# Performance work log

Hardware: AMD Instinct MI355X
Metric: run time of the kernel (lower is better)

## Reference

```python
import jax, jax.numpy as jnp
import numpy as np

EMB = 1024
HEAD = 64

def setup_inputs() -> dict:
    key = jax.random.key(0)
    kx, kq, kk, kv = jax.random.split(key, 4)
    x = jax.random.normal(kx, (8, 2048, EMB), dtype=jnp.float32)
    # nn.Linear(emb, head, bias=False): y = x @ W.T, W: [head, emb]. Store as [emb, head].
    s = 1.0 / np.sqrt(EMB)
    Wq = jax.random.uniform(kq, (EMB, HEAD), jnp.float32, -s, s)
    Wk = jax.random.uniform(kk, (EMB, HEAD), jnp.float32, -s, s)
    Wv = jax.random.uniform(kv, (EMB, HEAD), jnp.float32, -s, s)
    return {"x": x, "Wq": Wq, "Wk": Wk, "Wv": Wv}

def reference(x, Wq, Wk, Wv):
    B, T, C = x.shape
    q = x @ Wq  # [B,T,H]
    k = x @ Wk
    v = x @ Wv
    # NOTE: original scales by emb_size C, not head_size.
    wei = jnp.einsum('bth,bsh->bts', q, k) / jnp.sqrt(jnp.asarray(C, x.dtype))
    causal = jnp.tril(jnp.ones((T, T), dtype=bool))
    wei = jnp.where(causal, wei, -jnp.inf)
    wei = jax.nn.softmax(wei, axis=-1)
    return jnp.einsum('bts,bsh->bth', wei, v)
```

## Files before the change

### kernel.cpp

```cpp
#include <hip/hip_runtime.h>
#include <hip/hip_bf16.h>

typedef __bf16 bf16_t;
typedef __bf16 bf16x8 __attribute__((ext_vector_type(8)));
typedef __bf16 bf16x4 __attribute__((ext_vector_type(4)));
typedef float  f32x4  __attribute__((ext_vector_type(4)));

#define MFMA_BF16(A, B, C) __builtin_amdgcn_mfma_f32_16x16x32_bf16((A), (B), (C), 0, 0, 0)

#define BATCH 8
#define SEQ   2048
#define EMB   1024
#define HEAD  64

typedef __attribute__((address_space(3))) void as3_void;
typedef const __attribute__((address_space(1))) void as1_void;
#define GLOAD_LDS16(g, l) \
  __builtin_amdgcn_global_load_lds((as1_void*)(g), (as3_void*)(l), 16, 0, 0)

__global__ __launch_bounds__(256) void wtrans_kernel(
    const float* __restrict__ Wq, const float* __restrict__ Wk,
    const float* __restrict__ Wv, bf16_t* __restrict__ WT)
{
  __shared__ float tile[64][65];
  const int m  = blockIdx.x >> 4;
  const int kt = blockIdx.x & 15;
  const float* W = (m == 0) ? Wq : (m == 1) ? Wk : Wv;
  const float scale = (m == 0) ? 0.045084219f : 1.0f;
  const int k0 = kt * 64;

  #pragma unroll
  for (int i = 0; i < 16; ++i) {
    int idx = i * 256 + threadIdx.x;
    int kk = idx >> 6, n = idx & 63;
    tile[kk][n] = W[(size_t)(k0 + kk) * HEAD + n];
  }
  __syncthreads();
  #pragma unroll
  for (int i = 0; i < 16; ++i) {
    int idx = i * 256 + threadIdx.x;
    int n = idx >> 6, kk = idx & 63;
    WT[((size_t)m * HEAD + n) * EMB + k0 + kk] = (bf16_t)(tile[kk][n] * scale);
  }
}

#define A_BYTES 16384
#define B_BYTES 24576
#define BUF_BYTES 40960

__global__ __launch_bounds__(512, 1) void qkv_kernel(
    const float* __restrict__ x, const bf16_t* __restrict__ WT,
    bf16_t* __restrict__ qo, bf16_t* __restrict__ ko, bf16_t* __restrict__ vT)
{
  __shared__ char lds[4 * BUF_BYTES];

  const int tid  = threadIdx.x;
  const int lane = tid & 63;
  const int wave = tid >> 6;
  const int l15 = lane & 15, l4 = lane >> 4;
  const int wm = wave >> 2, wn = wave & 3;
  const int rowbase = blockIdx.x * 64;
  const int phase = (blockIdx.x >> 3) & 15;

  const int a_rsub = lane >> 4;
  const int b_rsub = lane >> 3;
  const int b_koff = ((lane & 7) * 16) ^ (b_rsub << 4);

  const int aswz = (l15 & 7) << 5;
  const int bswz = (l15 & 7) << 4;

  f32x4 acc[2][3];
  #pragma unroll
  for (int m = 0; m < 2; ++m)
    #pragma unroll
    for (int n = 0; n < 3; ++n) acc[m][n] = (f32x4){0.f, 0.f, 0.f, 0.f};

#define STAGE(t)                                                               \
  {                                                                            \
    char* buf = lds + ((t) & 3) * BUF_BYTES;                                   \
    const int tp = ((t) + phase) & 15;                                         \
    _Pragma("unroll")                                                          \
    for (int j = 0; j < 2; ++j) {                                              \
      const int g = 2 * wave + j;                                              \
      const int koff = (l15 * 16) ^ ((((j) << 2) | a_rsub) << 5);              \
      const char* src = (const char*)x + (size_t)(rowbase + 4 * g + a_rsub)    \
                        * 4096 + (size_t)tp * 256 + koff;                      \
      GLOAD_LDS16(src, buf + g * 1024);                                        \
    }                                                                          \
    _Pragma("unroll")                                                          \
    for (int j = 0; j < 3; ++j) {                                              \
      const int g = 3 * wave + j;                                              \
      const char* src = (const char*)WT + (size_t)(8 * g + b_rsub) * 2048      \
                        + (size_t)tp * 128 + b_koff;                           \
      GLOAD_LDS16(src, buf + A_BYTES + g * 1024);                              \
    }                                                                          \
  }

#define COMPUTE(t)                                                             \
  {                                                                            \
    const char* Ab = lds + ((t) & 3) * BUF_BYTES;                              \
    const char* Bb = Ab + A_BYTES;                                             \
    _Pragma("unroll")                                                          \
    for (int ks = 0; ks < 2; ++ks) {                                           \
      bf16x8 afr[2];                                                           \
      _Pragma("unroll")                                                        \
      for (int m = 0; m < 2; ++m) {                                            \
        const int R = wm * 32 + m * 16 + l15;                                  \
        const char* rp = Ab + R * 256 + ((ks * 128 + l4 * 32) ^ aswz);         \
        f32x4 p0 = *(const f32x4*)(rp);                                        \
        f32x4 p1 = *(const f32x4*)(rp + 16);                                   \
        bf16x8 a;                                                              \
        a[0] = (bf16_t)p0.x; a[1] = (bf16_t)p0.y;                              \
        a[2] = (bf16_t)p0.z; a[3] = (bf16_t)p0.w;                              \
        a[4] = (bf16_t)p1.x; a[5] = (bf16_t)p1.y;                              \
        a[6] = (bf16_t)p1.z; a[7] = (bf16_t)p1.w;                              \
        afr[m] = a;                                                            \
      }                                                                        \
      _Pragma("unroll")                                                        \
      for (int n = 0; n < 3; ++n) {                                            \
        const int Rb = wn * 48 + n * 16 + l15;                                 \
        bf16x8 b = *(const bf16x8*)(Bb + Rb * 128 + ((ks * 64 + l4 * 16) ^ bswz)); \
        acc[0][n] = MFMA_BF16(afr[0], b, acc[0][n]);                           \
        acc[1][n] = MFMA_BF16(afr[1], b, acc[1][n]);                           \
      }                                                                        \
    }                                                                          \
  }

  STAGE(0); STAGE(1); STAGE(2);
  asm volatile("s_waitcnt vmcnt(10)" ::: "memory");
  __builtin_amdgcn_s_barrier();

  for (int t = 0; t < 13; ++t) {
    COMPUTE(t);
    STAGE(t + 3);
    asm volatile("s_waitcnt vmcnt(10)" ::: "memory");
    __builtin_amdgcn_s_barrier();
  }
  COMPUTE(13);
  asm volatile("s_waitcnt vmcnt(5)" ::: "memory");
  __builtin_amdgcn_s_barrier();
  COMPUTE(14);
  asm volatile("s_waitcnt vmcnt(0)" ::: "memory");
  __builtin_amdgcn_s_barrier();
  COMPUTE(15);
#undef STAGE
#undef COMPUTE

  #pragma unroll
  for (int n = 0; n < 3; ++n) {
    const int col = wn * 48 + n * 16;
    #pragma unroll
    for (int m = 0; m < 2; ++m) {
      const int r0 = rowbase + wm * 32 + m * 16 + l4 * 4;
      if (col < 64) {
        #pragma unroll
        for (int i = 0; i < 4; ++i)
          qo[(size_t)(r0 + i) * HEAD + col + l15] = (bf16_t)acc[m][n][i];
      } else if (col < 128) {
        #pragma unroll
        for (int i = 0; i < 4; ++i)
          ko[(size_t)(r0 + i) * HEAD + col - 64 + l15] = (bf16_t)acc[m][n][i];
      } else {
        const int h = col - 128 + l15;
        bf16x4 pk;
        #pragma unroll
        for (int i = 0; i < 4; ++i) pk[i] = (bf16_t)acc[m][n][i];
        *(bf16x4*)(vT + ((size_t)(r0 >> 11) * HEAD + h) * SEQ + (r0 & 2047)) = pk;
      }
    }
  }
}

__global__ __launch_bounds__(512, 1) void attn_kernel(
    const bf16_t* __restrict__ q, const bf16_t* __restrict__ k,
    const bf16_t* __restrict__ vT, float* __restrict__ out)
{
  __shared__ bf16_t P[8][16][72];
  __shared__ float olds[8][16][65];
  __shared__ float lsums[8][16];
  const int lane = threadIdx.x & 63;
  const int wave = threadIdx.x >> 6;
  const int l15 = lane & 15, l4 = lane >> 4;
  const int batch = blockIdx.x & 7;
  const int pair  = blockIdx.x >> 3;
  const int side  = wave >> 2;
  const int wsub  = wave & 3;
  const int strip = side ? (127 - pair) : pair;
  const int qrow  = strip * 16;
  const int ntiles = (qrow >> 6) + 1;

  const bf16_t* kb = k  + (size_t)batch * SEQ * HEAD;
  const bf16_t* vb = vT + (size_t)batch * HEAD * SEQ;
  const bf16_t* qb = q  + ((size_t)batch * SEQ + qrow) * HEAD;

  const bf16x8 aq0 = *(const bf16x8*)(qb + (size_t)l15 * HEAD + l4 * 8);
  const bf16x8 aq1 = *(const bf16x8*)(qb + (size_t)l15 * HEAD + 32 + l4 * 8);

  f32x4 o[4];
  #pragma unroll
  for (int i = 0; i < 4; ++i) o[i] = (f32x4){0.f, 0.f, 0.f, 0.f};
  float lsum[4] = {0.f, 0.f, 0.f, 0.f};

  for (int t = wsub; t < ntiles; t += 4) {
    const int kv0 = t * 64;

    f32x4 s[4];
    #pragma unroll
    for (int nf = 0; nf < 4; ++nf) s[nf] = (f32x4){0.f, 0.f, 0.f, 0.f};
    __builtin_amdgcn_s_setprio(1);
    #pragma unroll
    for (int nf = 0; nf < 4; ++nf) {
      const bf16_t* kp = kb + (size_t)(kv0 + nf * 16 + l15) * HEAD + l4 * 8;
      bf16x8 b0 = *(const bf16x8*)kp;
      bf16x8 b1 = *(const bf16x8*)(kp + 32);
      s[nf] = MFMA_BF16(aq0, b0, s[nf]);
      s[nf] = MFMA_BF16(aq1, b1, s[nf]);
    }
    __builtin_amdgcn_s_setprio(0);

    const bool diag = (t == ntiles - 1);
    #pragma unroll
    for (int nf = 0; nf < 4; ++nf) {
      #pragma unroll
      for (int i2 = 0; i2 < 4; ++i2) {
        float e = exp2f(s[nf][i2]);
        if (diag) {
          const int col = kv0 + nf * 16 + l15;
          const int row = qrow + l4 * 4 + i2;
          e = (col <= row) ? e : 0.f;
        }
        lsum[i2] += e;
        P[wave][l4 * 4 + i2][nf * 16 + l15] = (bf16_t)e;
      }
    }

    bf16x8 v0[4], v1[4];
    #pragma unroll
    for (int nf = 0; nf < 4; ++nf) {
      const bf16_t* vp = vb + (size_t)(nf * 16 + l15) * SEQ + kv0 + l4 * 8;
      v0[nf] = *(const bf16x8*)vp;
      v1[nf] = *(const bf16x8*)(vp + 32);
    }
    asm volatile("s_waitcnt lgkmcnt(0)" ::: "memory");

    bf16x8 ap0 = *(const bf16x8*)&P[wave][l15][l4 * 8];
    bf16x8 ap1 = *(const bf16x8*)&P[wave][l15][32 + l4 * 8];
    __builtin_amdgcn_s_setprio(1);
    #pragma unroll
    for (int nf = 0; nf < 4; ++nf) {
      o[nf] = MFMA_BF16(ap0, v0[nf], o[nf]);
      o[nf] = MFMA_BF16(ap1, v1[nf], o[nf]);
    }
    __builtin_amdgcn_s_setprio(0);
  }

  #pragma unroll
  for (int i = 0; i < 4; ++i) {
    float v = lsum[i];
    v += __shfl_xor(v, 1);
    v += __shfl_xor(v, 2);
    v += __shfl_xor(v, 4);
    v += __shfl_xor(v, 8);
    if (l15 == 0) lsums[wave][l4 * 4 + i] = v;
  }
  #pragma unroll
  for (int nf = 0; nf < 4; ++nf)
    #pragma unroll
    for (int i = 0; i < 4; ++i)
      olds[wave][l4 * 4 + i][nf * 16 + l15] = o[nf][i];
  __syncthreads();

  {
    const int g  = threadIdx.x >> 8;
    const int tt = threadIdx.x & 255;
    const int r = tt >> 4, c0 = tt & 15;
    const int sstrip = g ? (127 - pair) : pair;
    const int w0 = g * 4;
    const float s = lsums[w0][r] + lsums[w0+1][r] + lsums[w0+2][r] + lsums[w0+3][r];
    const float rinv = 1.0f / s;
    float* ob = out + ((size_t)batch * SEQ + sstrip * 16 + r) * HEAD;
    #pragma unroll
    for (int j = 0; j < 4; ++j) {
      const int c = c0 + 16 * j;
      float v = olds[w0][r][c] + olds[w0+1][r][c] + olds[w0+2][r][c] + olds[w0+3][r][c];
      ob[c] = v * rinv;
    }
  }
}

extern "C" void kernel_launch(void* const* d_in, const int* in_sizes, int n_in,
                              void* d_out, int out_size, void* d_ws, size_t ws_size,
                              hipStream_t stream)
{
  const float* x  = (const float*)d_in[0];
  const float* Wq = (const float*)d_in[1];
  const float* Wk = (const float*)d_in[2];
  const float* Wv = (const float*)d_in[3];
  float* out = (float*)d_out;

  const size_t SZ_QKV = (size_t)BATCH * SEQ * HEAD * sizeof(bf16_t);
  if (ws_size < 3 * SZ_QKV + (size_t)192 * EMB * sizeof(bf16_t)) return;
  char* ws = (char*)d_ws;
  bf16_t* qo = (bf16_t*)(ws);
  bf16_t* ko = (bf16_t*)(ws + SZ_QKV);
  bf16_t* vT = (bf16_t*)(ws + 2 * SZ_QKV);
  bf16_t* WT = (bf16_t*)(ws + 3 * SZ_QKV);

  wtrans_kernel<<<dim3(48),  dim3(256), 0, stream>>>(Wq, Wk, Wv, WT);
  qkv_kernel  <<<dim3(256), dim3(512), 0, stream>>>(x, WT, qo, ko, vT);
  attn_kernel <<<dim3(512), dim3(512), 0, stream>>>(qo, ko, vT, out);
}
```

Before: 56.57 us.

## Share K tiles across waves via triple-buffered LDS and drop split-KV reduction

The attention kernel now gives each block four consecutive query strips, one per wave, and each wave walks every KV tile itself. K tiles are staged into a swizzled, triple-buffered LDS ring with global_load_lds, so the four waves share one K load per tile. The old split-KV scheme with cross-wave LDS reduction and the front/back strip pairing is removed. Output is normalised and written straight from registers. This cuts redundant K global traffic and the reduction step, but each wave's KV loop becomes serial and longer. Without pairing, blocks become strongly imbalanced, and only 256 blocks of 4 waves are launched, which lowers occupancy.

```diff
diff --git a/kernel.cpp b/kernel.cpp
--- a/kernel.cpp
+++ b/kernel.cpp
@@ -171,23 +171,20 @@
   }
 }
 
-__global__ __launch_bounds__(512, 1) void attn_kernel(
+__global__ __launch_bounds__(256) void attn_kernel(
     const bf16_t* __restrict__ q, const bf16_t* __restrict__ k,
     const bf16_t* __restrict__ vT, float* __restrict__ out)
 {
-  __shared__ bf16_t P[8][16][72];
-  __shared__ float olds[8][16][65];
-  __shared__ float lsums[8][16];
+  __shared__ char kbuf[3][8192];
+  __shared__ bf16_t P[4][16][72];
   const int lane = threadIdx.x & 63;
   const int wave = threadIdx.x >> 6;
   const int l15 = lane & 15, l4 = lane >> 4;
   const int batch = blockIdx.x & 7;
-  const int pair  = blockIdx.x >> 3;
-  const int side  = wave >> 2;
-  const int wsub  = wave & 3;
-  const int strip = side ? (127 - pair) : pair;
+  const int u = (int)(blockIdx.x >> 3);
+  const int strip = 4 * u + wave;
   const int qrow  = strip * 16;
-  const int ntiles = (qrow >> 6) + 1;
+  const int ntiles = u + 1;
 
   const bf16_t* kb = k  + (size_t)batch * SEQ * HEAD;
   const bf16_t* vb = vT + (size_t)batch * HEAD * SEQ;
@@ -196,13 +193,34 @@
   const bf16x8 aq0 = *(const bf16x8*)(qb + (size_t)l15 * HEAD + l4 * 8);
   const bf16x8 aq1 = *(const bf16x8*)(qb + (size_t)l15 * HEAD + 32 + l4 * 8);
 
+  const int b_rsub = lane >> 3;
+  const int b_koff = ((lane & 7) * 16) ^ (b_rsub << 4);
+  const int kswz = (l15 & 7) << 4;
+
+#define KSTAGE(t)                                                              \
+  {                                                                            \
+    char* buf = kbuf[(t) % 3];                                                 \
+    _Pragma("unroll")                                                          \
+    for (int j = 0; j < 2; ++j) {                                              \
+      const int g = 2 * wave + j;                                              \
+      const char* src = (const char*)kb + (size_t)((t) * 64 + 8 * g + b_rsub)  \
+                        * 128 + b_koff;                                        \
+      GLOAD_LDS16(src, buf + g * 1024);                                        \
+    }                                                                          \
+  }
+
   f32x4 o[4];
   #pragma unroll
   for (int i = 0; i < 4; ++i) o[i] = (f32x4){0.f, 0.f, 0.f, 0.f};
   float lsum[4] = {0.f, 0.f, 0.f, 0.f};
 
-  for (int t = wsub; t < ntiles; t += 4) {
+  KSTAGE(0); KSTAGE(1);
+  asm volatile("s_waitcnt vmcnt(2)" ::: "memory");
+  __builtin_amdgcn_s_barrier();
+
+  for (int t = 0; t < ntiles; ++t) {
     const int kv0 = t * 64;
+    const char* Kb = kbuf[t % 3];
 
     f32x4 s[4];
     #pragma unroll
@@ -210,13 +228,23 @@
     __builtin_amdgcn_s_setprio(1);
     #pragma unroll
     for (int nf = 0; nf < 4; ++nf) {
-      const bf16_t* kp = kb + (size_t)(kv0 + nf * 16 + l15) * HEAD + l4 * 8;
-      bf16x8 b0 = *(const bf16x8*)kp;
-      bf16x8 b1 = *(const bf16x8*)(kp + 32);
+      const char* kr = (const char*)Kb + (nf * 16 + l15) * 128;
+      bf16x8 b0 = *(const bf16x8*)(kr + ((l4 * 16) ^ kswz));
+      bf16x8 b1 = *(const bf16x8*)(kr + ((64 + l4 * 16) ^ kswz));
       s[nf] = MFMA_BF16(aq0, b0, s[nf]);
       s[nf] = MFMA_BF16(aq1, b1, s[nf]);
     }
     __builtin_amdgcn_s_setprio(0);
+
+    bf16x8 v0[4], v1[4];
+    #pragma unroll
+    for (int nf = 0; nf < 4; ++nf) {
+      const bf16_t* vp = vb + (size_t)(nf * 16 + l15) * SEQ + kv0 + l4 * 8;
+      v0[nf] = *(const bf16x8*)vp;
+      v1[nf] = *(const bf16x8*)(vp + 32);
+    }
+
+    if (t + 2 < ntiles) KSTAGE(t + 2);
 
     const bool diag = (t == ntiles - 1);
     #pragma unroll
@@ -234,17 +262,11 @@
       }
     }
 
-    bf16x8 v0[4], v1[4];
-    #pragma unroll
-    for (int nf = 0; nf < 4; ++nf) {
-      const bf16_t* vp = vb + (size_t)(nf * 16 + l15) * SEQ + kv0 + l4 * 8;
-      v0[nf] = *(const bf16x8*)vp;
-      v1[nf] = *(const bf16x8*)(vp + 32);
-    }
-    asm volatile("s_waitcnt lgkmcnt(0)" ::: "memory");
-
     bf16x8 ap0 = *(const bf16x8*)&P[wave][l15][l4 * 8];
     bf16x8 ap1 = *(const bf16x8*)&P[wave][l15][32 + l4 * 8];
+
+    asm volatile("s_waitcnt vmcnt(2)" ::: "memory");
+
     __builtin_amdgcn_s_setprio(1);
     #pragma unroll
     for (int nf = 0; nf < 4; ++nf) {
@@ -252,7 +274,10 @@
       o[nf] = MFMA_BF16(ap1, v1[nf], o[nf]);
     }
     __builtin_amdgcn_s_setprio(0);
-  }
+
+    __builtin_amdgcn_s_barrier();
+  }
+#undef KSTAGE
 
   #pragma unroll
   for (int i = 0; i < 4; ++i) {
@@ -261,31 +286,14 @@
     v += __shfl_xor(v, 2);
     v += __shfl_xor(v, 4);
     v += __shfl_xor(v, 8);
-    if (l15 == 0) lsums[wave][l4 * 4 + i] = v;
-  }
+    lsum[i] = 1.0f / v;
+  }
+  float* ob = out + ((size_t)batch * SEQ + qrow) * HEAD;
   #pragma unroll
   for (int nf = 0; nf < 4; ++nf)
     #pragma unroll
     for (int i = 0; i < 4; ++i)
-      olds[wave][l4 * 4 + i][nf * 16 + l15] = o[nf][i];
-  __syncthreads();
-
-  {
-    const int g  = threadIdx.x >> 8;
-    const int tt = threadIdx.x & 255;
-    const int r = tt >> 4, c0 = tt & 15;
-    const int sstrip = g ? (127 - pair) : pair;
-    const int w0 = g * 4;
-    const float s = lsums[w0][r] + lsums[w0+1][r] + lsums[w0+2][r] + lsums[w0+3][r];
-    const float rinv = 1.0f / s;
-    float* ob = out + ((size_t)batch * SEQ + sstrip * 16 + r) * HEAD;
-    #pragma unroll
-    for (int j = 0; j < 4; ++j) {
-      const int c = c0 + 16 * j;
-      float v = olds[w0][r][c] + olds[w0+1][r][c] + olds[w0+2][r][c] + olds[w0+3][r][c];
-      ob[c] = v * rinv;
-    }
-  }
+      ob[(size_t)(l4 * 4 + i) * HEAD + nf * 16 + l15] = o[nf][i] * lsum[i];
 }
 
 extern "C" void kernel_launch(void* const* d_in, const int* in_sizes, int n_in,
@@ -308,5 +316,5 @@
 
   wtrans_kernel<<<dim3(48),  dim3(256), 0, stream>>>(Wq, Wk, Wv, WT);
   qkv_kernel  <<<dim3(256), dim3(512), 0, stream>>>(x, WT, qo, ko, vT);
-  attn_kernel <<<dim3(512), dim3(512), 0, stream>>>(qo, ko, vT, out);
+  attn_kernel <<<dim3(256), dim3(256), 0, stream>>>(qo, ko, vT, out);
 }
```

New measurement: 73.22 us. 1.29x slower.
